# Kernel tuning notes

Measured on AMD Instinct MI355X. Metric: run time of the kernel, lower is better.

The kernel has to match this reference:

```python
import jax, jax.numpy as jnp
import numpy as np

H = 1024          # hidden_size
M = 512           # moe_intermediate_size
E = 16            # n_routed_experts
TOP_K = 4         # num_experts_per_tok
N_GROUP = 4
TOPK_GROUP = 2
SCALE = 2.5       # routed_scaling_factor
B, S = 2, 1024


def setup_inputs() -> dict:
    key = jax.random.key(0)
    ks = jax.random.split(key, 9)
    sc_h = 1.0 / np.sqrt(H)
    sc_m = 1.0 / np.sqrt(M)
    return {
        "hidden_states": jax.random.normal(ks[0], (B, S, H), jnp.float32),
        "gate_kernel": jax.random.normal(ks[1], (H, E), jnp.float32) * sc_h,
        "gate_bias": jax.random.normal(ks[2], (E,), jnp.float32) * 0.01,
        "w_gate": jax.random.normal(ks[3], (E, H, M), jnp.float32) * sc_h,
        "w_up": jax.random.normal(ks[4], (E, H, M), jnp.float32) * sc_h,
        "w_down": jax.random.normal(ks[5], (E, M, H), jnp.float32) * sc_m,
        "sw_gate": jax.random.normal(ks[6], (H, 2 * M), jnp.float32) * sc_h,
        "sw_up": jax.random.normal(ks[7], (H, 2 * M), jnp.float32) * sc_h,
        "sw_down": jax.random.normal(ks[8], (2 * M, H), jnp.float32) * (1.0 / np.sqrt(2 * M)),
    }


def _gate(x2d, gate_kernel, gate_bias):
    # x2d: [N, H]
    n = x2d.shape[0]
    logits = jnp.dot(x2d.astype(jnp.float32), gate_kernel.astype(jnp.float32))  # [N, E]
    scores = jax.nn.sigmoid(logits)
    scores_for_choice = scores + gate_bias  # noaux_tc correction bias
    # group-limited top-k: sum of top-2 scores per group
    group_scores = scores_for_choice.reshape(n, N_GROUP, E // N_GROUP)
    top2 = jax.lax.top_k(group_scores, k=2)[0]
    group_sum = jnp.sum(top2, axis=-1)                       # [N, G]
    group_idx = jax.lax.top_k(group_sum, k=TOPK_GROUP)[1]    # [N, topk_group]
    group_mask = jnp.zeros_like(group_sum).at[jnp.arange(n)[:, None], group_idx].set(1.0)
    score_mask = jnp.repeat(group_mask[:, :, None], E // N_GROUP, axis=2).reshape(n, E)
    masked_scores = jnp.where(score_mask > 0, scores_for_choice, 0.0)
    topk_weight, topk_idx = jax.lax.top_k(masked_scores, k=TOP_K)
    # norm_topk_prob
    topk_weight = topk_weight / (jnp.sum(topk_weight, axis=-1, keepdims=True) + 1e-20)
    topk_weight = topk_weight * SCALE
    return topk_idx, topk_weight


def reference(hidden_states, gate_kernel, gate_bias, w_gate, w_up, w_down,
              sw_gate, sw_up, sw_down):
    orig_shape = hidden_states.shape
    x = hidden_states.reshape(-1, orig_shape[-1])  # [N, H]
    topk_idx, topk_weight = _gate(x, gate_kernel, gate_bias)
    # combine weight per (token, expert): sum_k (topk_idx==e) * topk_weight
    onehot = (topk_idx[:, :, None] == jnp.arange(E)[None, None, :]).astype(topk_weight.dtype)
    combine = jnp.einsum('nke,nk->ne', onehot, topk_weight)  # [N, E]
    # dense per-expert MLP (faithful to moe_infer which runs every expert)
    g = jnp.einsum('nh,ehm->enm', x, w_gate)   # [E, N, M]
    u = jnp.einsum('nh,ehm->enm', x, w_up)
    inter = jax.nn.silu(g) * u
    y_e = jnp.einsum('enm,emh->enh', inter, w_down)          # [E, N, H]
    y = jnp.einsum('ne,enh->nh', combine, y_e)               # [N, H]
    # shared-expert path
    shared = jnp.dot(jax.nn.silu(jnp.dot(x, sw_gate)) * jnp.dot(x, sw_up), sw_down)
    return (y + shared).reshape(orig_shape)
```

## Files before the change

### kernel.cpp

```cpp
#include <hip/hip_runtime.h>
#include <hip/hip_bf16.h>
#include <cstdint>

#define HID    1024
#define MID    512
#define NEXP   16
#define NTOKS  2048
#define TOPKE  4
#define RSCALE 2.5f
#define CSTR   16

typedef __attribute__((ext_vector_type(8))) short  bf16x8;
typedef __attribute__((ext_vector_type(8))) ushort u16x8;
typedef __attribute__((ext_vector_type(4))) float  f32x4;

__device__ __forceinline__ ushort f2bf(float f){
  unsigned u = __float_as_uint(f);
  u += 0x7fffu + ((u >> 16) & 1u);
  return (ushort)(u >> 16);
}
__device__ __forceinline__ float bf2f(ushort h){ return __uint_as_float(((unsigned)h) << 16); }

#define GLD16(g, l) __builtin_amdgcn_global_load_lds( \
    (const __attribute__((address_space(1))) unsigned int*)(g), \
    (__attribute__((address_space(3))) unsigned int*)(l), 16, 0, 0)

__global__ __launch_bounds__(256) void k_route(const float* __restrict__ x,
                                               const float* __restrict__ gk,
                                               const float* __restrict__ gb,
                                               int* __restrict__ counts,
                                               int* __restrict__ tidx,
                                               float* __restrict__ tw)
{
  __shared__ float sc[16][16];
  __shared__ int lcnt[NEXP];
  const int tid = threadIdx.x;
  const int tl  = tid >> 4;
  const int e   = tid & 15;
  const int t   = blockIdx.x * 16 + tl;

  float acc = 0.f;
  const float* xr = x + (size_t)t * HID;
  for (int h = 0; h < HID; h += 4){
    f32x4 xv = *reinterpret_cast<const f32x4*>(xr + h);
    acc += xv[0] * gk[(h+0)*NEXP + e];
    acc += xv[1] * gk[(h+1)*NEXP + e];
    acc += xv[2] * gk[(h+2)*NEXP + e];
    acc += xv[3] * gk[(h+3)*NEXP + e];
  }
  sc[tl][e] = 1.f / (1.f + expf(-acc)) + gb[e];
  if (tid < NEXP) lcnt[tid] = 0;
  __syncthreads();

  if (tid < 16){
    const int tt = blockIdx.x * 16 + tid;
    float s4[NEXP];
    #pragma unroll
    for (int i = 0; i < NEXP; ++i) s4[i] = sc[tid][i];
    float gs[4];
    #pragma unroll
    for (int g = 0; g < 4; ++g){
      float m1 = -1e30f, m2 = -1e30f;
      #pragma unroll
      for (int j = 0; j < 4; ++j){
        float v = s4[g*4+j];
        if (v > m1){ m2 = m1; m1 = v; } else if (v > m2){ m2 = v; }
      }
      gs[g] = m1 + m2;
    }
    int g1 = 0;
    for (int g = 1; g < 4; ++g) if (gs[g] > gs[g1]) g1 = g;
    int g2 = -1;
    for (int g = 0; g < 4; ++g){
      if (g == g1) continue;
      if (g2 < 0 || gs[g] > gs[g2]) g2 = g;
    }
    float ms[NEXP];
    #pragma unroll
    for (int i = 0; i < NEXP; ++i){
      int g = i >> 2;
      ms[i] = (g == g1 || g == g2) ? s4[i] : 0.0f;
    }
    bool used[NEXP];
    #pragma unroll
    for (int i = 0; i < NEXP; ++i) used[i] = false;
    int sel[TOPKE]; float val[TOPKE]; float denom = 0.f;
    #pragma unroll
    for (int k = 0; k < TOPKE; ++k){
      int be = -1; float bv = -1e30f;
      for (int i = 0; i < NEXP; ++i){
        if (used[i]) continue;
        if (ms[i] > bv){ bv = ms[i]; be = i; }
      }
      used[be] = true; sel[k] = be; val[k] = bv; denom += bv;
    }
    float inv = RSCALE / (denom + 1e-20f);
    #pragma unroll
    for (int k = 0; k < TOPKE; ++k){
      tidx[tt*TOPKE + k] = sel[k];
      tw  [tt*TOPKE + k] = val[k] * inv;
      atomicAdd(&lcnt[sel[k]], 1);
    }
  }
  __syncthreads();
  if (tid < NEXP && lcnt[tid]) atomicAdd(&counts[tid * CSTR], lcnt[tid]);
}

__global__ __launch_bounds__(256) void k_place(const int* __restrict__ tidx,
                                               const float* __restrict__ tw,
                                               const int* __restrict__ counts,
                                               int* __restrict__ cursor,
                                               int* __restrict__ tlist,
                                               float* __restrict__ wlist,
                                               int* __restrict__ pos)
{
  __shared__ int lcnt[NEXP];
  __shared__ int lbase[NEXP];
  __shared__ int soff[NEXP];
  const int tid = threadIdx.x;
  const int t = blockIdx.x * 256 + tid;
  if (tid < NEXP){
    lcnt[tid] = 0;
    int s = 0;
    for (int i = 0; i < tid; ++i) s += counts[i * CSTR];
    soff[tid] = s;
  }
  __syncthreads();
  int sel[TOPKE]; float w4[TOPKE]; int ls[TOPKE];
  #pragma unroll
  for (int k = 0; k < TOPKE; ++k){
    sel[k] = tidx[t*TOPKE + k];
    w4[k]  = tw[t*TOPKE + k];
    ls[k]  = atomicAdd(&lcnt[sel[k]], 1);
  }
  __syncthreads();
  if (tid < NEXP) lbase[tid] = atomicAdd(&cursor[tid * CSTR], lcnt[tid]);
  __syncthreads();
  #pragma unroll
  for (int k = 0; k < TOPKE; ++k){
    int p = soff[sel[k]] + lbase[sel[k]] + ls[k];
    tlist[p] = t;
    wlist[p] = w4[k];
    pos[t*TOPKE + k] = p;
  }
}

__global__ __launch_bounds__(256) void k_cvt(const float* __restrict__ in,
                                             ushort* __restrict__ out, int n8)
{
  int i = blockIdx.x * 256 + threadIdx.x;
  if (i >= n8) return;
  f32x4 a = *reinterpret_cast<const f32x4*>(in + (size_t)i*8);
  f32x4 b = *reinterpret_cast<const f32x4*>(in + (size_t)i*8 + 4);
  u16x8 o;
  o[0]=f2bf(a[0]); o[1]=f2bf(a[1]); o[2]=f2bf(a[2]); o[3]=f2bf(a[3]);
  o[4]=f2bf(b[0]); o[5]=f2bf(b[1]); o[6]=f2bf(b[2]); o[7]=f2bf(b[3]);
  *reinterpret_cast<u16x8*>(out + (size_t)i*8) = o;
}

__device__ __forceinline__ void tr_body(const float* __restrict__ in,
                                        ushort* __restrict__ out, int K, int N)
{
  const int kb = blockIdx.y * 64, nb = blockIdx.x * 64;
  __shared__ ushort T[64 * 68];
  const int t = threadIdx.x;
  const int r = t >> 4, c4 = (t & 15) * 4;
  #pragma unroll
  for (int i = 0; i < 4; ++i){
    f32x4 v = *reinterpret_cast<const f32x4*>(in + (size_t)(kb + r + i*16) * N + nb + c4);
    #pragma unroll
    for (int j = 0; j < 4; ++j)
      T[(c4 + j) * 68 + r + i*16] = f2bf(v[j]);
  }
  __syncthreads();
  const int n  = t >> 2;
  const int kb8 = t & 3;
  #pragma unroll
  for (int i = 0; i < 2; ++i){
    int k8 = kb8 + i * 4;
    ushort4 lo = *reinterpret_cast<const ushort4*>(&T[n * 68 + k8 * 8]);
    ushort4 hi = *reinterpret_cast<const ushort4*>(&T[n * 68 + k8 * 8 + 4]);
    u16x8 o;
    o[0]=lo.x; o[1]=lo.y; o[2]=lo.z; o[3]=lo.w;
    o[4]=hi.x; o[5]=hi.y; o[6]=hi.z; o[7]=hi.w;
    *reinterpret_cast<u16x8*>(out + (size_t)(nb + n) * K + kb + k8 * 8) = o;
  }
}

__global__ __launch_bounds__(256) void k_trS(const float* __restrict__ a,
                                             const float* __restrict__ b,
                                             const float* __restrict__ c,
                                             ushort* __restrict__ oa,
                                             ushort* __restrict__ ob,
                                             ushort* __restrict__ oc)
{
  const int z = blockIdx.z;
  const float* in = (z == 0) ? a : (z == 1) ? b : c;
  ushort* out     = (z == 0) ? oa : (z == 1) ? ob : oc;
  tr_body(in, out, 1024, 1024);
}

__global__ __launch_bounds__(256) void k_trR(const float* __restrict__ a,
                                             const float* __restrict__ b,
                                             ushort* __restrict__ oa,
                                             ushort* __restrict__ ob,
                                             int K, int N, int split)
{
  const int z = blockIdx.z;
  const int e = z % split;
  const float* in = ((z < split) ? a : b) + (size_t)e * K * N;
  ushort* out     = ((z < split) ? oa : ob) + (size_t)e * K * N;
  tr_body(in, out, K, N);
}

__global__ __launch_bounds__(256) void k_mm0(
    const ushort* __restrict__ xb,
    ushort* __restrict__ i_s, ushort* __restrict__ i_r,
    const ushort* __restrict__ swgT, const ushort* __restrict__ swuT,
    const ushort* __restrict__ wgT,  const ushort* __restrict__ wuT,
    const int* __restrict__ counts, const int* __restrict__ tlist)
{
  const int z = blockIdx.z;
  const bool routed = (z >= 2);
  const int e = z - 2;
  const int mbase = blockIdx.y * 128;
  int cnt = NTOKS, aoff = 0;
  if (routed){
    cnt = counts[e * CSTR];
    if (mbase >= cnt) return;
    for (int i = 0; i < e; ++i) aoff += counts[i * CSTR];
  }
  const int Nout    = routed ? 512 : 1024;
  const int colBase = routed ? (blockIdx.x * 64) : (z * 512 + blockIdx.x * 64);
  const ushort* Bg = routed ? (wgT + (size_t)e * MID * HID) : swgT;
  const ushort* Bu = routed ? (wuT + (size_t)e * MID * HID) : swuT;
  ushort* O = routed ? i_r : i_s;

  __shared__ __align__(16) ushort Sh[16384];

  const int tid = threadIdx.x;
  const int l   = tid & 63;
  const int w   = tid >> 6;
  const int wm  = w >> 1;
  const int wn  = w & 1;

  const int rl     = l >> 3;
  const int srcOff = 8 * ((l & 7) ^ rl);

  const ushort* srcP[8];
  #pragma unroll
  for (int j = 0; j < 8; ++j){
    int g = w * 8 + j;
    const ushort* p;
    if (g < 16){
      int ar = mbase + g * 8 + rl;
      if (routed){
        int s = aoff + (ar < cnt ? ar : cnt - 1);
        p = xb + (size_t)tlist[s] * HID;
      } else p = xb + (size_t)ar * HID;
    } else if (g < 24){
      p = Bg + (size_t)(colBase + (g - 16) * 8 + rl) * HID;
    } else {
      p = Bu + (size_t)(colBase + (g - 24) * 8 + rl) * HID;
    }
    srcP[j] = p + srcOff;
  }

  f32x4 accg[4][2], accu[4][2];
  #pragma unroll
  for (int i = 0; i < 4; ++i)
    #pragma unroll
    for (int j = 0; j < 2; ++j){
      accg[i][j] = (f32x4){0.f,0.f,0.f,0.f};
      accu[i][j] = (f32x4){0.f,0.f,0.f,0.f};
    }

  const int fr  = l & 15;
  const int ko  = l >> 4;
  const int swz = (fr & 7) << 4;

  for (int kt = 0; kt < 16; ++kt){
    const int ke = kt * 64;
    #pragma unroll
    for (int j = 0; j < 8; ++j)
      GLD16(srcP[j] + ke, (ushort*)Sh + (w*8 + j) * 512 + l * 8);
    __syncthreads();
    #pragma unroll
    for (int ks = 0; ks < 2; ++ks){
      const int co = ks * 64 + ko * 16;
      bf16x8 af[4], bg[2], bu[2];
      #pragma unroll
      for (int mf = 0; mf < 4; ++mf)
        af[mf] = *reinterpret_cast<const bf16x8*>(
            (const char*)Sh + (wm*64 + mf*16 + fr) * 128 + (co ^ swz));
      #pragma unroll
      for (int nf = 0; nf < 2; ++nf){
        int cc = wn*32 + nf*16 + fr;
        bg[nf] = *reinterpret_cast<const bf16x8*>(
            (const char*)Sh + 16384 + cc * 128 + (co ^ swz));
        bu[nf] = *reinterpret_cast<const bf16x8*>(
            (const char*)Sh + 24576 + cc * 128 + (co ^ swz));
      }
      #pragma unroll
      for (int mf = 0; mf < 4; ++mf)
        #pragma unroll
        for (int nf = 0; nf < 2; ++nf){
          accg[mf][nf] = __builtin_amdgcn_mfma_f32_16x16x32_bf16(af[mf], bg[nf], accg[mf][nf], 0, 0, 0);
          accu[mf][nf] = __builtin_amdgcn_mfma_f32_16x16x32_bf16(af[mf], bu[nf], accu[mf][nf], 0, 0, 0);
        }
    }
    __syncthreads();
  }

  const int ccol = l & 15;
  const int crow = (l >> 4) * 4;
  #pragma unroll
  for (int mf = 0; mf < 4; ++mf){
    #pragma unroll
    for (int r_ = 0; r_ < 4; ++r_){
      const int arel = wm*64 + mf*16 + crow + r_ + mbase;
      if (routed && arel >= cnt) continue;
      size_t row = routed ? (size_t)(aoff + arel) : (size_t)arel;
      #pragma unroll
      for (int nf = 0; nf < 2; ++nf){
        int col = colBase + wn*32 + nf*16 + ccol;
        float g = accg[mf][nf][r_];
        float u = accu[mf][nf][r_];
        float s = g / (1.f + expf(-g));
        O[row * Nout + col] = f2bf(s * u);
      }
    }
  }
}

__global__ __launch_bounds__(256) void k_mm1(
    const ushort* __restrict__ i_s, const ushort* __restrict__ i_r,
    const ushort* __restrict__ swdT, const ushort* __restrict__ wdT,
    ushort* __restrict__ y_s, ushort* __restrict__ y_r,
    const int* __restrict__ counts, const float* __restrict__ wlist)
{
  const int z = blockIdx.z;
  const bool routed = (z > 0);
  const int e = z - 1;
  const int Kd = routed ? MID : HID;
  const int mbase = blockIdx.y * 128;
  const int nbase = blockIdx.x * 128;
  int cnt = NTOKS, aoff = 0;
  if (routed){
    cnt = counts[e * CSTR];
    if (mbase >= cnt) return;
    for (int i = 0; i < e; ++i) aoff += counts[i * CSTR];
  }
  const ushort* A = routed ? i_r : i_s;
  const ushort* B = routed ? (wdT + (size_t)e * HID * MID) : swdT;

  __shared__ __align__(16) ushort Sh[16384];

  const int tid = threadIdx.x;
  const int l   = tid & 63;
  const int w   = tid >> 6;
  const int wm  = w >> 1;
  const int wn  = w & 1;

  const int rl     = l >> 3;
  const int srcOff = 8 * ((l & 7) ^ rl);

  const ushort* srcP[8];
  #pragma unroll
  for (int j = 0; j < 8; ++j){
    int g = w * 8 + j;
    const ushort* p;
    if (g < 16){
      int ar = mbase + g * 8 + rl;
      if (routed){
        int s = aoff + (ar < cnt ? ar : cnt - 1);
        p = A + (size_t)s * Kd;
      } else p = A + (size_t)ar * Kd;
    } else {
      p = B + (size_t)(nbase + (g - 16) * 8 + rl) * Kd;
    }
    srcP[j] = p + srcOff;
  }

  f32x4 acc[4][4];
  #pragma unroll
  for (int i = 0; i < 4; ++i)
    #pragma unroll
    for (int j = 0; j < 4; ++j)
      acc[i][j] = (f32x4){0.f,0.f,0.f,0.f};

  const int fr  = l & 15;
  const int ko  = l >> 4;
  const int swz = (fr & 7) << 4;
  const int nk  = Kd >> 6;

  for (int kt = 0; kt < nk; ++kt){
    const int ke = kt * 64;
    #pragma unroll
    for (int j = 0; j < 8; ++j)
      GLD16(srcP[j] + ke, (ushort*)Sh + (w*8 + j) * 512 + l * 8);
    __syncthreads();
    #pragma unroll
    for (int ks = 0; ks < 2; ++ks){
      const int co = ks * 64 + ko * 16;
      bf16x8 af[4], bf[4];
      #pragma unroll
      for (int mf = 0; mf < 4; ++mf)
        af[mf] = *reinterpret_cast<const bf16x8*>(
            (const char*)Sh + (wm*64 + mf*16 + fr) * 128 + (co ^ swz));
      #pragma unroll
      for (int nf = 0; nf < 4; ++nf)
        bf[nf] = *reinterpret_cast<const bf16x8*>(
            (const char*)Sh + 16384 + (wn*64 + nf*16 + fr) * 128 + (co ^ swz));
      #pragma unroll
      for (int mf = 0; mf < 4; ++mf)
        #pragma unroll
        for (int nf = 0; nf < 4; ++nf)
          acc[mf][nf] = __builtin_amdgcn_mfma_f32_16x16x32_bf16(af[mf], bf[nf], acc[mf][nf], 0, 0, 0);
    }
    __syncthreads();
  }

  const int ccol = l & 15;
  const int crow = (l >> 4) * 4;
  #pragma unroll
  for (int mf = 0; mf < 4; ++mf){
    #pragma unroll
    for (int r_ = 0; r_ < 4; ++r_){
      const int arel = wm*64 + mf*16 + crow + r_ + mbase;
      if (routed && arel >= cnt) continue;
      if (!routed){
        #pragma unroll
        for (int nf = 0; nf < 4; ++nf){
          int col = nbase + wn*64 + nf*16 + ccol;
          y_s[(size_t)arel * HID + col] = f2bf(acc[mf][nf][r_]);
        }
      } else {
        int s = aoff + arel;
        float wgt = wlist[s];
        #pragma unroll
        for (int nf = 0; nf < 4; ++nf){
          int col = nbase + wn*64 + nf*16 + ccol;
          y_r[(size_t)s * HID + col] = f2bf(wgt * acc[mf][nf][r_]);
        }
      }
    }
  }
}

__global__ __launch_bounds__(256) void k_comb(const ushort* __restrict__ y_s,
                                              const ushort* __restrict__ y_r,
                                              const int* __restrict__ pos,
                                              float* __restrict__ out)
{
  const int t  = blockIdx.x * 2 + (threadIdx.x >> 7);
  const int c8 = (threadIdx.x & 127) * 8;
  const int* pp = pos + t * TOPKE;
  u16x8 vs = *reinterpret_cast<const u16x8*>(y_s + (size_t)t * HID + c8);
  float s[8];
  #pragma unroll
  for (int j = 0; j < 8; ++j) s[j] = bf2f(vs[j]);
  #pragma unroll
  for (int k = 0; k < TOPKE; ++k){
    int p = pp[k];
    u16x8 vr = *reinterpret_cast<const u16x8*>(y_r + (size_t)p * HID + c8);
    #pragma unroll
    for (int j = 0; j < 8; ++j) s[j] += bf2f(vr[j]);
  }
  f32x4 o0 = (f32x4){s[0],s[1],s[2],s[3]};
  f32x4 o1 = (f32x4){s[4],s[5],s[6],s[7]};
  *reinterpret_cast<f32x4*>(out + (size_t)t * HID + c8)     = o0;
  *reinterpret_cast<f32x4*>(out + (size_t)t * HID + c8 + 4) = o1;
}

extern "C" void kernel_launch(void* const* d_in, const int* in_sizes, int n_in,
                              void* d_out, int out_size, void* d_ws, size_t ws_size,
                              hipStream_t stream)
{
  const float* x   = (const float*)d_in[0];
  const float* gk  = (const float*)d_in[1];
  const float* gb  = (const float*)d_in[2];
  const float* wg  = (const float*)d_in[3];
  const float* wu  = (const float*)d_in[4];
  const float* wd  = (const float*)d_in[5];
  const float* swg = (const float*)d_in[6];
  const float* swu = (const float*)d_in[7];
  const float* swd = (const float*)d_in[8];
  float* out = (float*)d_out;
  char* ws = (char*)d_ws;

  const size_t MB = 1ull << 20;
  int*    counts = (int*)(ws + 0);
  int*    cursor = (int*)(ws + 2048);
  int*    tidx   = (int*)(ws + 8192);
  float*  tw     = (float*)(ws + 49152);
  int*    tlist  = (int*)(ws + 90112);
  float*  wlist  = (float*)(ws + 131072);
  int*    pos    = (int*)(ws + 163840);
  ushort* xb     = (ushort*)(ws + 1*MB);
  ushort* swgT   = (ushort*)(ws + 5*MB);
  ushort* swuT   = (ushort*)(ws + 7*MB);
  ushort* swdT   = (ushort*)(ws + 9*MB);
  ushort* wgT    = (ushort*)(ws + 11*MB);
  ushort* wuT    = (ushort*)(ws + 27*MB);
  ushort* wdT    = (ushort*)(ws + 43*MB);
  ushort* i_s    = (ushort*)(ws + 59*MB);
  ushort* i_r    = (ushort*)(ws + 63*MB);
  ushort* y_r    = (ushort*)(ws + 11*MB);
  ushort* y_s    = (ushort*)(ws + 27*MB);

  hipMemsetAsync(ws, 0, 4096, stream);
  k_route<<<128, 256, 0, stream>>>(x, gk, gb, counts, tidx, tw);
  k_place<<<NTOKS/256, 256, 0, stream>>>(tidx, tw, counts, cursor, tlist, wlist, pos);

  k_cvt<<<1024, 256, 0, stream>>>(x, xb, 262144);
  k_trS<<<dim3(16,16,3),  256, 0, stream>>>(swg, swu, swd, swgT, swuT, swdT);
  k_trR<<<dim3( 8,16,32), 256, 0, stream>>>(wg, wu, wgT, wuT, 1024, 512, 16);
  k_trR<<<dim3(16, 8,16), 256, 0, stream>>>(wd, wd, wdT, wdT, 512, 1024, 16);

  k_mm0<<<dim3(8,16,18), 256, 0, stream>>>(xb, i_s, i_r, swgT, swuT, wgT, wuT,
                                           counts, tlist);
  k_mm1<<<dim3(8,16,17), 256, 0, stream>>>(i_s, i_r, swdT, wdT, y_s, y_r,
                                           counts, wlist);
  k_comb<<<NTOKS/2, 256, 0, stream>>>(y_s, y_r, pos, out);
}
```

Measured before the change: 169.2 us.

## Fuse weight transposes into GEMM launches to overlap conversion with compute

Merges the activation cast and shared-weight transposes into one prep kernel. It then folds the routed gate/up weight transposes into the shared-expert GEMM launch, and the down-weight transpose into the routed GEMM launch, splitting the old combined mm0 kernel into shared and routed variants. This cuts the number of launches and lets bandwidth-bound transpose blocks run alongside compute-bound GEMM blocks. The cost is heterogeneous blocks within each grid and a stricter ordering dependency between the split kernels.

```diff
diff --git a/kernel.cpp b/kernel.cpp
--- a/kernel.cpp
+++ b/kernel.cpp
@@ -145,24 +145,11 @@
   }
 }
 
-__global__ __launch_bounds__(256) void k_cvt(const float* __restrict__ in,
-                                             ushort* __restrict__ out, int n8)
-{
-  int i = blockIdx.x * 256 + threadIdx.x;
-  if (i >= n8) return;
-  f32x4 a = *reinterpret_cast<const f32x4*>(in + (size_t)i*8);
-  f32x4 b = *reinterpret_cast<const f32x4*>(in + (size_t)i*8 + 4);
-  u16x8 o;
-  o[0]=f2bf(a[0]); o[1]=f2bf(a[1]); o[2]=f2bf(a[2]); o[3]=f2bf(a[3]);
-  o[4]=f2bf(b[0]); o[5]=f2bf(b[1]); o[6]=f2bf(b[2]); o[7]=f2bf(b[3]);
-  *reinterpret_cast<u16x8*>(out + (size_t)i*8) = o;
-}
-
-__device__ __forceinline__ void tr_body(const float* __restrict__ in,
-                                        ushort* __restrict__ out, int K, int N)
-{
-  const int kb = blockIdx.y * 64, nb = blockIdx.x * 64;
-  __shared__ ushort T[64 * 68];
+__device__ __forceinline__ void tr_tile(const float* __restrict__ in,
+                                        ushort* __restrict__ out,
+                                        int K, int N, int kb, int nb,
+                                        ushort* __restrict__ T)
+{
   const int t = threadIdx.x;
   const int r = t >> 4, c4 = (t & 15) * 4;
   #pragma unroll
@@ -173,7 +160,7 @@
       T[(c4 + j) * 68 + r + i*16] = f2bf(v[j]);
   }
   __syncthreads();
-  const int n  = t >> 2;
+  const int n   = t >> 2;
   const int kb8 = t & 3;
   #pragma unroll
   for (int i = 0; i < 2; ++i){
@@ -187,56 +174,53 @@
   }
 }
 
-__global__ __launch_bounds__(256) void k_trS(const float* __restrict__ a,
-                                             const float* __restrict__ b,
-                                             const float* __restrict__ c,
-                                             ushort* __restrict__ oa,
-                                             ushort* __restrict__ ob,
-                                             ushort* __restrict__ oc)
-{
+__global__ __launch_bounds__(256) void k_prep(
+    const float* __restrict__ x, ushort* __restrict__ xb,
+    const float* __restrict__ swg, const float* __restrict__ swu,
+    const float* __restrict__ swd,
+    ushort* __restrict__ swgT, ushort* __restrict__ swuT,
+    ushort* __restrict__ swdT)
+{
+  __shared__ ushort T[64 * 68];
   const int z = blockIdx.z;
-  const float* in = (z == 0) ? a : (z == 1) ? b : c;
-  ushort* out     = (z == 0) ? oa : (z == 1) ? ob : oc;
-  tr_body(in, out, 1024, 1024);
-}
-
-__global__ __launch_bounds__(256) void k_trR(const float* __restrict__ a,
-                                             const float* __restrict__ b,
-                                             ushort* __restrict__ oa,
-                                             ushort* __restrict__ ob,
-                                             int K, int N, int split)
-{
+  if (z < 3){
+    const float* in = (z == 0) ? swg : (z == 1) ? swu : swd;
+    ushort* out     = (z == 0) ? swgT : (z == 1) ? swuT : swdT;
+    tr_tile(in, out, 1024, 1024, blockIdx.y * 64, blockIdx.x * 64, T);
+    return;
+  }
+  const int blk = blockIdx.y * 16 + blockIdx.x;
+  #pragma unroll
+  for (int j = 0; j < 4; ++j){
+    int i = blk * 1024 + j * 256 + threadIdx.x;
+    f32x4 a = *reinterpret_cast<const f32x4*>(x + (size_t)i*8);
+    f32x4 b = *reinterpret_cast<const f32x4*>(x + (size_t)i*8 + 4);
+    u16x8 o;
+    o[0]=f2bf(a[0]); o[1]=f2bf(a[1]); o[2]=f2bf(a[2]); o[3]=f2bf(a[3]);
+    o[4]=f2bf(b[0]); o[5]=f2bf(b[1]); o[6]=f2bf(b[2]); o[7]=f2bf(b[3]);
+    *reinterpret_cast<u16x8*>(xb + (size_t)i*8) = o;
+  }
+}
+
+__global__ __launch_bounds__(256) void k_mm0s(
+    const ushort* __restrict__ xb, ushort* __restrict__ i_s,
+    const ushort* __restrict__ swgT, const ushort* __restrict__ swuT,
+    const float* __restrict__ wg, const float* __restrict__ wu,
+    ushort* __restrict__ wgT, ushort* __restrict__ wuT)
+{
+  __shared__ __align__(16) ushort Sh[16384];
   const int z = blockIdx.z;
-  const int e = z % split;
-  const float* in = ((z < split) ? a : b) + (size_t)e * K * N;
-  ushort* out     = ((z < split) ? oa : ob) + (size_t)e * K * N;
-  tr_body(in, out, K, N);
-}
-
-__global__ __launch_bounds__(256) void k_mm0(
-    const ushort* __restrict__ xb,
-    ushort* __restrict__ i_s, ushort* __restrict__ i_r,
-    const ushort* __restrict__ swgT, const ushort* __restrict__ swuT,
-    const ushort* __restrict__ wgT,  const ushort* __restrict__ wuT,
-    const int* __restrict__ counts, const int* __restrict__ tlist)
-{
-  const int z = blockIdx.z;
-  const bool routed = (z >= 2);
-  const int e = z - 2;
-  const int mbase = blockIdx.y * 128;
-  int cnt = NTOKS, aoff = 0;
-  if (routed){
-    cnt = counts[e * CSTR];
-    if (mbase >= cnt) return;
-    for (int i = 0; i < e; ++i) aoff += counts[i * CSTR];
-  }
-  const int Nout    = routed ? 512 : 1024;
-  const int colBase = routed ? (blockIdx.x * 64) : (z * 512 + blockIdx.x * 64);
-  const ushort* Bg = routed ? (wgT + (size_t)e * MID * HID) : swgT;
-  const ushort* Bu = routed ? (wuT + (size_t)e * MID * HID) : swuT;
-  ushort* O = routed ? i_r : i_s;
-
-  __shared__ __align__(16) ushort Sh[16384];
+  if (z >= 2){
+    const bool isU = (z >= 18);
+    const int e = isU ? (z - 18) : (z - 2);
+    const float* in = (isU ? wu : wg) + (size_t)e * HID * MID;
+    ushort* out     = (isU ? wuT : wgT) + (size_t)e * HID * MID;
+    tr_tile(in, out, 1024, 512, blockIdx.y * 64, blockIdx.x * 64, Sh);
+    return;
+  }
+
+  const int mbase   = blockIdx.y * 128;
+  const int colBase = z * 512 + blockIdx.x * 64;
 
   const int tid = threadIdx.x;
   const int l   = tid & 63;
@@ -254,14 +238,11 @@
     const ushort* p;
     if (g < 16){
       int ar = mbase + g * 8 + rl;
-      if (routed){
-        int s = aoff + (ar < cnt ? ar : cnt - 1);
-        p = xb + (size_t)tlist[s] * HID;
-      } else p = xb + (size_t)ar * HID;
+      p = xb + (size_t)ar * HID;
     } else if (g < 24){
-      p = Bg + (size_t)(colBase + (g - 16) * 8 + rl) * HID;
+      p = swgT + (size_t)(colBase + (g - 16) * 8 + rl) * HID;
     } else {
-      p = Bu + (size_t)(colBase + (g - 24) * 8 + rl) * HID;
+      p = swuT + (size_t)(colBase + (g - 24) * 8 + rl) * HID;
     }
     srcP[j] = p + srcOff;
   }
@@ -318,16 +299,133 @@
   for (int mf = 0; mf < 4; ++mf){
     #pragma unroll
     for (int r_ = 0; r_ < 4; ++r_){
-      const int arel = wm*64 + mf*16 + crow + r_ + mbase;
-      if (routed && arel >= cnt) continue;
-      size_t row = routed ? (size_t)(aoff + arel) : (size_t)arel;
+      const int row = wm*64 + mf*16 + crow + r_ + mbase;
       #pragma unroll
       for (int nf = 0; nf < 2; ++nf){
         int col = colBase + wn*32 + nf*16 + ccol;
         float g = accg[mf][nf][r_];
         float u = accu[mf][nf][r_];
         float s = g / (1.f + expf(-g));
-        O[row * Nout + col] = f2bf(s * u);
+        i_s[(size_t)row * 1024 + col] = f2bf(s * u);
+      }
+    }
+  }
+}
+
+__global__ __launch_bounds__(256) void k_mm0r(
+    const ushort* __restrict__ xb, ushort* __restrict__ i_r,
+    const ushort* __restrict__ wgT, const ushort* __restrict__ wuT,
+    const float* __restrict__ wd, ushort* __restrict__ wdT,
+    const int* __restrict__ counts, const int* __restrict__ tlist)
+{
+  __shared__ __align__(16) ushort Sh[16384];
+  const int z = blockIdx.z;
+  if (z >= 16){
+    const int e = z - 16;
+    tr_tile(wd + (size_t)e * MID * HID, wdT + (size_t)e * MID * HID,
+            512, 1024, blockIdx.x * 64, blockIdx.y * 64, Sh);
+    return;
+  }
+
+  const int e = z;
+  const int mbase = blockIdx.y * 128;
+  const int cnt = counts[e * CSTR];
+  if (mbase >= cnt) return;
+  int aoff = 0;
+  for (int i = 0; i < e; ++i) aoff += counts[i * CSTR];
+
+  const int colBase = blockIdx.x * 64;
+  const ushort* Bg = wgT + (size_t)e * MID * HID;
+  const ushort* Bu = wuT + (size_t)e * MID * HID;
+
+  const int tid = threadIdx.x;
+  const int l   = tid & 63;
+  const int w   = tid >> 6;
+  const int wm  = w >> 1;
+  const int wn  = w & 1;
+
+  const int rl     = l >> 3;
+  const int srcOff = 8 * ((l & 7) ^ rl);
+
+  const ushort* srcP[8];
+  #pragma unroll
+  for (int j = 0; j < 8; ++j){
+    int g = w * 8 + j;
+    const ushort* p;
+    if (g < 16){
+      int ar = mbase + g * 8 + rl;
+      int s = aoff + (ar < cnt ? ar : cnt - 1);
+      p = xb + (size_t)tlist[s] * HID;
+    } else if (g < 24){
+      p = Bg + (size_t)(colBase + (g - 16) * 8 + rl) * HID;
+    } else {
+      p = Bu + (size_t)(colBase + (g - 24) * 8 + rl) * HID;
+    }
+    srcP[j] = p + srcOff;
+  }
+
+  f32x4 accg[4][2], accu[4][2];
+  #pragma unroll
+  for (int i = 0; i < 4; ++i)
+    #pragma unroll
+    for (int j = 0; j < 2; ++j){
+      accg[i][j] = (f32x4){0.f,0.f,0.f,0.f};
+      accu[i][j] = (f32x4){0.f,0.f,0.f,0.f};
+    }
+
+  const int fr  = l & 15;
+  const int ko  = l >> 4;
+  const int swz = (fr & 7) << 4;
+
+  for (int kt = 0; kt < 16; ++kt){
+    const int ke = kt * 64;
+    #pragma unroll
+    for (int j = 0; j < 8; ++j)
+      GLD16(srcP[j] + ke, (ushort*)Sh + (w*8 + j) * 512 + l * 8);
+    __syncthreads();
+    #pragma unroll
+    for (int ks = 0; ks < 2; ++ks){
+      const int co = ks * 64 + ko * 16;
+      bf16x8 af[4], bg[2], bu[2];
+      #pragma unroll
+      for (int mf = 0; mf < 4; ++mf)
+        af[mf] = *reinterpret_cast<const bf16x8*>(
+            (const char*)Sh + (wm*64 + mf*16 + fr) * 128 + (co ^ swz));
+      #pragma unroll
+      for (int nf = 0; nf < 2; ++nf){
+        int cc = wn*32 + nf*16 + fr;
+        bg[nf] = *reinterpret_cast<const bf16x8*>(
+            (const char*)Sh + 16384 + cc * 128 + (co ^ swz));
+        bu[nf] = *reinterpret_cast<const bf16x8*>(
+            (const char*)Sh + 24576 + cc * 128 + (co ^ swz));
+      }
+      #pragma unroll
+      for (int mf = 0; mf < 4; ++mf)
+        #pragma unroll
+        for (int nf = 0; nf < 2; ++nf){
+          accg[mf][nf] = __builtin_amdgcn_mfma_f32_16x16x32_bf16(af[mf], bg[nf], accg[mf][nf], 0, 0, 0);
+          accu[mf][nf] = __builtin_amdgcn_mfma_f32_16x16x32_bf16(af[mf], bu[nf], accu[mf][nf], 0, 0, 0);
+        }
+    }
+    __syncthreads();
+  }
+
+  const int ccol = l & 15;
+  const int crow = (l >> 4) * 4;
+  #pragma unroll
+  for (int mf = 0; mf < 4; ++mf){
+    #pragma unroll
+    for (int r_ = 0; r_ < 4; ++r_){
+      const int arel = wm*64 + mf*16 + crow + r_ + mbase;
+      if (arel >= cnt) continue;
+      size_t row = (size_t)(aoff + arel);
+      #pragma unroll
+      for (int nf = 0; nf < 2; ++nf){
+        int col = colBase + wn*32 + nf*16 + ccol;
+        float g = accg[mf][nf][r_];
+        float u = accu[mf][nf][r_];
+        float s = g / (1.f + expf(-g));
+        i_r[row * 512 + col] = f2bf(s * u);
       }
     }
   }
@@ -513,13 +611,10 @@
   k_route<<<128, 256, 0, stream>>>(x, gk, gb, counts, tidx, tw);
   k_place<<<NTOKS/256, 256, 0, stream>>>(tidx, tw, counts, cursor, tlist, wlist, pos);
 
-  k_cvt<<<1024, 256, 0, stream>>>(x, xb, 262144);
-  k_trS<<<dim3(16,16,3),  256, 0, stream>>>(swg, swu, swd, swgT, swuT, swdT);
-  k_trR<<<dim3( 8,16,32), 256, 0, stream>>>(wg, wu, wgT, wuT, 1024, 512, 16);
-  k_trR<<<dim3(16, 8,16), 256, 0, stream>>>(wd, wd, wdT, wdT, 512, 1024, 16);
-
-  k_mm0<<<dim3(8,16,18), 256, 0, stream>>>(xb, i_s, i_r, swgT, swuT, wgT, wuT,
-                                           counts, tlist);
+  k_prep<<<dim3(16,16,4), 256, 0, stream>>>(x, xb, swg, swu, swd, swgT, swuT, swdT);
+
+  k_mm0s<<<dim3(8,16,34), 256, 0, stream>>>(xb, i_s, swgT, swuT, wg, wu, wgT, wuT);
+  k_mm0r<<<dim3(8,16,32), 256, 0, stream>>>(xb, i_r, wgT, wuT, wd, wdT, counts, tlist);
   k_mm1<<<dim3(8,16,17), 256, 0, stream>>>(i_s, i_r, swdT, wdT, y_s, y_r,
                                            counts, wlist);
   k_comb<<<NTOKS/2, 256, 0, stream>>>(y_s, y_r, pos, out);
```

New measurement: 167.9 us. No clear change (-0.8%).

## Fuse preprocessing kernels and overlap down-weight transpose with first GEMM

Applied to the files above, without the earlier changes.

Merges the routing gate, bf16 conversion of activations, and shared/routed gate-up weight transposes into one multi-role kernel indexed by blockIdx.z. The down-projection weight transpose is moved into extra z-slices of the first GEMM kernel so it runs alongside the matmul blocks. This removes several kernel launches and the idle tails between them, at the cost of more branchy, heterogeneous blocks within each launch.

```diff
diff --git a/kernel.cpp b/kernel.cpp
--- a/kernel.cpp
+++ b/kernel.cpp
@@ -25,85 +25,150 @@
     (const __attribute__((address_space(1))) unsigned int*)(g), \
     (__attribute__((address_space(3))) unsigned int*)(l), 16, 0, 0)
 
-__global__ __launch_bounds__(256) void k_route(const float* __restrict__ x,
-                                               const float* __restrict__ gk,
-                                               const float* __restrict__ gb,
-                                               int* __restrict__ counts,
-                                               int* __restrict__ tidx,
-                                               float* __restrict__ tw)
-{
+__device__ __forceinline__ void tr_tile(const float* __restrict__ in,
+                                        ushort* __restrict__ out,
+                                        int K, int N, int kb, int nb,
+                                        ushort* __restrict__ T)
+{
+  const int t = threadIdx.x;
+  const int r = t >> 4, c4 = (t & 15) * 4;
+  #pragma unroll
+  for (int i = 0; i < 4; ++i){
+    f32x4 v = *reinterpret_cast<const f32x4*>(in + (size_t)(kb + r + i*16) * N + nb + c4);
+    #pragma unroll
+    for (int j = 0; j < 4; ++j)
+      T[(c4 + j) * 68 + r + i*16] = f2bf(v[j]);
+  }
+  __syncthreads();
+  const int n   = t >> 2;
+  const int kb8 = t & 3;
+  #pragma unroll
+  for (int i = 0; i < 2; ++i){
+    int k8 = kb8 + i * 4;
+    ushort4 lo = *reinterpret_cast<const ushort4*>(&T[n * 68 + k8 * 8]);
+    ushort4 hi = *reinterpret_cast<const ushort4*>(&T[n * 68 + k8 * 8 + 4]);
+    u16x8 o;
+    o[0]=lo.x; o[1]=lo.y; o[2]=lo.z; o[3]=lo.w;
+    o[4]=hi.x; o[5]=hi.y; o[6]=hi.z; o[7]=hi.w;
+    *reinterpret_cast<u16x8*>(out + (size_t)(nb + n) * K + kb + k8 * 8) = o;
+  }
+}
+
+__global__ __launch_bounds__(256) void k_pre(
+    const float* __restrict__ x, ushort* __restrict__ xb,
+    const float* __restrict__ gk, const float* __restrict__ gb,
+    const float* __restrict__ swg, const float* __restrict__ swu,
+    const float* __restrict__ swd,
+    const float* __restrict__ wg, const float* __restrict__ wu,
+    ushort* __restrict__ swgT, ushort* __restrict__ swuT,
+    ushort* __restrict__ swdT,
+    ushort* __restrict__ wgT, ushort* __restrict__ wuT,
+    int* __restrict__ counts, int* __restrict__ tidx, float* __restrict__ tw)
+{
+  __shared__ ushort T[64 * 68];
   __shared__ float sc[16][16];
   __shared__ int lcnt[NEXP];
-  const int tid = threadIdx.x;
-  const int tl  = tid >> 4;
-  const int e   = tid & 15;
-  const int t   = blockIdx.x * 16 + tl;
-
-  float acc = 0.f;
-  const float* xr = x + (size_t)t * HID;
-  for (int h = 0; h < HID; h += 4){
-    f32x4 xv = *reinterpret_cast<const f32x4*>(xr + h);
-    acc += xv[0] * gk[(h+0)*NEXP + e];
-    acc += xv[1] * gk[(h+1)*NEXP + e];
-    acc += xv[2] * gk[(h+2)*NEXP + e];
-    acc += xv[3] * gk[(h+3)*NEXP + e];
-  }
-  sc[tl][e] = 1.f / (1.f + expf(-acc)) + gb[e];
-  if (tid < NEXP) lcnt[tid] = 0;
-  __syncthreads();
-
-  if (tid < 16){
-    const int tt = blockIdx.x * 16 + tid;
-    float s4[NEXP];
-    #pragma unroll
-    for (int i = 0; i < NEXP; ++i) s4[i] = sc[tid][i];
-    float gs[4];
-    #pragma unroll
-    for (int g = 0; g < 4; ++g){
-      float m1 = -1e30f, m2 = -1e30f;
-      #pragma unroll
-      for (int j = 0; j < 4; ++j){
-        float v = s4[g*4+j];
-        if (v > m1){ m2 = m1; m1 = v; } else if (v > m2){ m2 = v; }
-      }
-      gs[g] = m1 + m2;
-    }
-    int g1 = 0;
-    for (int g = 1; g < 4; ++g) if (gs[g] > gs[g1]) g1 = g;
-    int g2 = -1;
-    for (int g = 0; g < 4; ++g){
-      if (g == g1) continue;
-      if (g2 < 0 || gs[g] > gs[g2]) g2 = g;
-    }
-    float ms[NEXP];
-    #pragma unroll
-    for (int i = 0; i < NEXP; ++i){
-      int g = i >> 2;
-      ms[i] = (g == g1 || g == g2) ? s4[i] : 0.0f;
-    }
-    bool used[NEXP];
-    #pragma unroll
-    for (int i = 0; i < NEXP; ++i) used[i] = false;
-    int sel[TOPKE]; float val[TOPKE]; float denom = 0.f;
-    #pragma unroll
-    for (int k = 0; k < TOPKE; ++k){
-      int be = -1; float bv = -1e30f;
+  const int z = blockIdx.z;
+  const int bid = blockIdx.y * 8 + blockIdx.x;
+
+  if (z < 6){
+    const int m = z >> 1;
+    const float* in = (m == 0) ? swg : (m == 1) ? swu : swd;
+    ushort* out     = (m == 0) ? swgT : (m == 1) ? swuT : swdT;
+    tr_tile(in, out, 1024, 1024, blockIdx.y * 64, (z & 1) * 512 + blockIdx.x * 64, T);
+    return;
+  }
+  if (z < 38){
+    const bool isU = (z >= 22);
+    const int e = isU ? (z - 22) : (z - 6);
+    const float* in = (isU ? wu : wg) + (size_t)e * HID * MID;
+    ushort* out     = (isU ? wuT : wgT) + (size_t)e * HID * MID;
+    tr_tile(in, out, 1024, 512, blockIdx.y * 64, blockIdx.x * 64, T);
+    return;
+  }
+  if (z == 38){
+    #pragma unroll
+    for (int j = 0; j < 8; ++j){
+      int i = bid * 2048 + j * 256 + threadIdx.x;
+      f32x4 a = *reinterpret_cast<const f32x4*>(x + (size_t)i*8);
+      f32x4 b = *reinterpret_cast<const f32x4*>(x + (size_t)i*8 + 4);
+      u16x8 o;
+      o[0]=f2bf(a[0]); o[1]=f2bf(a[1]); o[2]=f2bf(a[2]); o[3]=f2bf(a[3]);
+      o[4]=f2bf(b[0]); o[5]=f2bf(b[1]); o[6]=f2bf(b[2]); o[7]=f2bf(b[3]);
+      *reinterpret_cast<u16x8*>(xb + (size_t)i*8) = o;
+    }
+    return;
+  }
+  {
+    const int tid = threadIdx.x;
+    const int tl  = tid >> 4;
+    const int e   = tid & 15;
+    const int t   = bid * 16 + tl;
+    float acc = 0.f;
+    const float* xr = x + (size_t)t * HID;
+    for (int h = 0; h < HID; h += 4){
+      f32x4 xv = *reinterpret_cast<const f32x4*>(xr + h);
+      acc += xv[0] * gk[(h+0)*NEXP + e];
+      acc += xv[1] * gk[(h+1)*NEXP + e];
+      acc += xv[2] * gk[(h+2)*NEXP + e];
+      acc += xv[3] * gk[(h+3)*NEXP + e];
+    }
+    sc[tl][e] = 1.f / (1.f + expf(-acc)) + gb[e];
+    if (tid < NEXP) lcnt[tid] = 0;
+    __syncthreads();
+    if (tid < 16){
+      const int tt = bid * 16 + tid;
+      float s4[NEXP];
+      #pragma unroll
+      for (int i = 0; i < NEXP; ++i) s4[i] = sc[tid][i];
+      float gs[4];
+      #pragma unroll
+      for (int g = 0; g < 4; ++g){
+        float m1 = -1e30f, m2 = -1e30f;
+        #pragma unroll
+        for (int j = 0; j < 4; ++j){
+          float v = s4[g*4+j];
+          if (v > m1){ m2 = m1; m1 = v; } else if (v > m2){ m2 = v; }
+        }
+        gs[g] = m1 + m2;
+      }
+      int g1 = 0;
+      for (int g = 1; g < 4; ++g) if (gs[g] > gs[g1]) g1 = g;
+      int g2 = -1;
+      for (int g = 0; g < 4; ++g){
+        if (g == g1) continue;
+        if (g2 < 0 || gs[g] > gs[g2]) g2 = g;
+      }
+      float ms[NEXP];
+      #pragma unroll
       for (int i = 0; i < NEXP; ++i){
-        if (used[i]) continue;
-        if (ms[i] > bv){ bv = ms[i]; be = i; }
-      }
-      used[be] = true; sel[k] = be; val[k] = bv; denom += bv;
-    }
-    float inv = RSCALE / (denom + 1e-20f);
-    #pragma unroll
-    for (int k = 0; k < TOPKE; ++k){
-      tidx[tt*TOPKE + k] = sel[k];
-      tw  [tt*TOPKE + k] = val[k] * inv;
-      atomicAdd(&lcnt[sel[k]], 1);
-    }
-  }
-  __syncthreads();
-  if (tid < NEXP && lcnt[tid]) atomicAdd(&counts[tid * CSTR], lcnt[tid]);
+        int g = i >> 2;
+        ms[i] = (g == g1 || g == g2) ? s4[i] : 0.0f;
+      }
+      bool used[NEXP];
+      #pragma unroll
+      for (int i = 0; i < NEXP; ++i) used[i] = false;
+      int sel[TOPKE]; float val[TOPKE]; float denom = 0.f;
+      #pragma unroll
+      for (int k = 0; k < TOPKE; ++k){
+        int be = -1; float bv = -1e30f;
+        for (int i = 0; i < NEXP; ++i){
+          if (used[i]) continue;
+          if (ms[i] > bv){ bv = ms[i]; be = i; }
+        }
+        used[be] = true; sel[k] = be; val[k] = bv; denom += bv;
+      }
+      float inv = RSCALE / (denom + 1e-20f);
+      #pragma unroll
+      for (int k = 0; k < TOPKE; ++k){
+        tidx[tt*TOPKE + k] = sel[k];
+        tw  [tt*TOPKE + k] = val[k] * inv;
+        atomicAdd(&lcnt[sel[k]], 1);
+      }
+    }
+    __syncthreads();
+    if (tid < NEXP && lcnt[tid]) atomicAdd(&counts[tid * CSTR], lcnt[tid]);
+  }
 }
 
 __global__ __launch_bounds__(256) void k_place(const int* __restrict__ tidx,
@@ -145,82 +210,23 @@
   }
 }
 
-__global__ __launch_bounds__(256) void k_cvt(const float* __restrict__ in,
-                                             ushort* __restrict__ out, int n8)
-{
-  int i = blockIdx.x * 256 + threadIdx.x;
-  if (i >= n8) return;
-  f32x4 a = *reinterpret_cast<const f32x4*>(in + (size_t)i*8);
-  f32x4 b = *reinterpret_cast<const f32x4*>(in + (size_t)i*8 + 4);
-  u16x8 o;
-  o[0]=f2bf(a[0]); o[1]=f2bf(a[1]); o[2]=f2bf(a[2]); o[3]=f2bf(a[3]);
-  o[4]=f2bf(b[0]); o[5]=f2bf(b[1]); o[6]=f2bf(b[2]); o[7]=f2bf(b[3]);
-  *reinterpret_cast<u16x8*>(out + (size_t)i*8) = o;
-}
-
-__device__ __forceinline__ void tr_body(const float* __restrict__ in,
-                                        ushort* __restrict__ out, int K, int N)
-{
-  const int kb = blockIdx.y * 64, nb = blockIdx.x * 64;
-  __shared__ ushort T[64 * 68];
-  const int t = threadIdx.x;
-  const int r = t >> 4, c4 = (t & 15) * 4;
-  #pragma unroll
-  for (int i = 0; i < 4; ++i){
-    f32x4 v = *reinterpret_cast<const f32x4*>(in + (size_t)(kb + r + i*16) * N + nb + c4);
-    #pragma unroll
-    for (int j = 0; j < 4; ++j)
-      T[(c4 + j) * 68 + r + i*16] = f2bf(v[j]);
-  }
-  __syncthreads();
-  const int n  = t >> 2;
-  const int kb8 = t & 3;
-  #pragma unroll
-  for (int i = 0; i < 2; ++i){
-    int k8 = kb8 + i * 4;
-    ushort4 lo = *reinterpret_cast<const ushort4*>(&T[n * 68 + k8 * 8]);
-    ushort4 hi = *reinterpret_cast<const ushort4*>(&T[n * 68 + k8 * 8 + 4]);
-    u16x8 o;
-    o[0]=lo.x; o[1]=lo.y; o[2]=lo.z; o[3]=lo.w;
-    o[4]=hi.x; o[5]=hi.y; o[6]=hi.z; o[7]=hi.w;
-    *reinterpret_cast<u16x8*>(out + (size_t)(nb + n) * K + kb + k8 * 8) = o;
-  }
-}
-
-__global__ __launch_bounds__(256) void k_trS(const float* __restrict__ a,
-                                             const float* __restrict__ b,
-                                             const float* __restrict__ c,
-                                             ushort* __restrict__ oa,
-                                             ushort* __restrict__ ob,
-                                             ushort* __restrict__ oc)
-{
-  const int z = blockIdx.z;
-  const float* in = (z == 0) ? a : (z == 1) ? b : c;
-  ushort* out     = (z == 0) ? oa : (z == 1) ? ob : oc;
-  tr_body(in, out, 1024, 1024);
-}
-
-__global__ __launch_bounds__(256) void k_trR(const float* __restrict__ a,
-                                             const float* __restrict__ b,
-                                             ushort* __restrict__ oa,
-                                             ushort* __restrict__ ob,
-                                             int K, int N, int split)
-{
-  const int z = blockIdx.z;
-  const int e = z % split;
-  const float* in = ((z < split) ? a : b) + (size_t)e * K * N;
-  ushort* out     = ((z < split) ? oa : ob) + (size_t)e * K * N;
-  tr_body(in, out, K, N);
-}
-
 __global__ __launch_bounds__(256) void k_mm0(
     const ushort* __restrict__ xb,
     ushort* __restrict__ i_s, ushort* __restrict__ i_r,
     const ushort* __restrict__ swgT, const ushort* __restrict__ swuT,
     const ushort* __restrict__ wgT,  const ushort* __restrict__ wuT,
+    const float* __restrict__ wd, ushort* __restrict__ wdT,
     const int* __restrict__ counts, const int* __restrict__ tlist)
 {
+  __shared__ __align__(16) ushort Sh[16384];
   const int z = blockIdx.z;
+  if (z >= 18){
+    const int e = z - 18;
+    tr_tile(wd + (size_t)e * MID * HID, wdT + (size_t)e * MID * HID,
+            512, 1024, blockIdx.x * 64, blockIdx.y * 64, Sh);
+    return;
+  }
+
   const bool routed = (z >= 2);
   const int e = z - 2;
   const int mbase = blockIdx.y * 128;
@@ -235,8 +241,6 @@
   const ushort* Bg = routed ? (wgT + (size_t)e * MID * HID) : swgT;
   const ushort* Bu = routed ? (wuT + (size_t)e * MID * HID) : swuT;
   ushort* O = routed ? i_r : i_s;
-
-  __shared__ __align__(16) ushort Sh[16384];
 
   const int tid = threadIdx.x;
   const int l   = tid & 63;
@@ -510,16 +514,13 @@
   ushort* y_s    = (ushort*)(ws + 27*MB);
 
   hipMemsetAsync(ws, 0, 4096, stream);
-  k_route<<<128, 256, 0, stream>>>(x, gk, gb, counts, tidx, tw);
+  k_pre<<<dim3(8,16,40), 256, 0, stream>>>(x, xb, gk, gb, swg, swu, swd, wg, wu,
+                                           swgT, swuT, swdT, wgT, wuT,
+                                           counts, tidx, tw);
   k_place<<<NTOKS/256, 256, 0, stream>>>(tidx, tw, counts, cursor, tlist, wlist, pos);
 
-  k_cvt<<<1024, 256, 0, stream>>>(x, xb, 262144);
-  k_trS<<<dim3(16,16,3),  256, 0, stream>>>(swg, swu, swd, swgT, swuT, swdT);
-  k_trR<<<dim3( 8,16,32), 256, 0, stream>>>(wg, wu, wgT, wuT, 1024, 512, 16);
-  k_trR<<<dim3(16, 8,16), 256, 0, stream>>>(wd, wd, wdT, wdT, 512, 1024, 16);
-
-  k_mm0<<<dim3(8,16,18), 256, 0, stream>>>(xb, i_s, i_r, swgT, swuT, wgT, wuT,
-                                           counts, tlist);
+  k_mm0<<<dim3(8,16,34), 256, 0, stream>>>(xb, i_s, i_r, swgT, swuT, wgT, wuT,
+                                           wd, wdT, counts, tlist);
   k_mm1<<<dim3(8,16,17), 256, 0, stream>>>(i_s, i_r, swdT, wdT, y_s, y_r,
                                            counts, wlist);
   k_comb<<<NTOKS/2, 256, 0, stream>>>(y_s, y_r, pos, out);
```

After: 167.9 us. About the same (-0.8%).
